# Kernel tuning notes

Hardware: AMD Instinct MI355X
Metric: run time of the kernel (lower is better)

## Reference

```python
import jax, jax.numpy as jnp
import numpy as np

N_E = 8192
E_DIM = 256
BETA = 0.25

def setup_inputs() -> dict:
    key = jax.random.key(0)
    k1, k2 = jax.random.split(key)
    z = jax.random.normal(k1, (2, E_DIM, 8, 32, 32), dtype=jnp.float32)
    # nn.Embedding init: uniform(-1/n_e, 1/n_e)
    codebook = jax.random.uniform(k2, (N_E, E_DIM), dtype=jnp.float32,
                                  minval=-1.0 / N_E, maxval=1.0 / N_E)
    return {"z": z, "codebook": codebook}

def reference(z, codebook):
    # b c d h w -> b d h w c
    z_t = jnp.transpose(z, (0, 2, 3, 4, 1))  # [B,D,H,W,C]
    zf = z_t.reshape(-1, E_DIM)               # [N, C]
    # squared-distance: ||z||^2 + ||e||^2 - 2 z.e^T
    d = (jnp.sum(zf * zf, axis=1, keepdims=True)
         + jnp.sum(codebook * codebook, axis=1)
         - 2.0 * jnp.matmul(zf, codebook.T))  # [N, n_e]
    idx = jnp.argmin(d, axis=1)                # [N]
    z_q = codebook[idx].reshape(z_t.shape)     # [B,D,H,W,C]
    sg = jax.lax.stop_gradient
    loss = jnp.mean((sg(z_q) - z_t) ** 2) + BETA * jnp.mean((z_q - sg(z_t)) ** 2)
    # straight-through estimator
    z_q_st = z_t + sg(z_q - z_t)
    z_q_out = jnp.transpose(z_q_st, (0, 4, 1, 2, 3))  # [B,C,D,H,W]
    # perplexity (no-grad stats)
    min_encodings = jax.nn.one_hot(idx, N_E, dtype=jnp.float32)  # [N, n_e]
    e_mean = jnp.mean(min_encodings, axis=0)
    perplexity = jnp.exp(-jnp.sum(e_mean * jnp.log(e_mean + 1e-10)))
    return (z_q_out, loss, perplexity, min_encodings, idx)
```

## Files before the change

### kernel.cpp

```cpp
#include <hip/hip_runtime.h>

typedef _Float16 half8 __attribute__((ext_vector_type(8)));
typedef float floatx4 __attribute__((ext_vector_type(4)));

#define DEVI __device__ __forceinline__
#define AS1 __attribute__((address_space(1)))
#define AS3 __attribute__((address_space(3)))
#define GLL(gp, lp) __builtin_amdgcn_global_load_lds((const AS1 void*)(gp), (AS3 void*)(lp), 16, 0, 0)
#define VM0 asm volatile("s_waitcnt vmcnt(0)" ::: "memory")
#define VM2 asm volatile("s_waitcnt vmcnt(2)" ::: "memory")
#define BAR __builtin_amdgcn_s_barrier()

namespace {
constexpr int C_   = 256;
constexpr int DHW_ = 8192;
constexpr int N_   = 16384;
constexpr int NE_  = 8192;
constexpr int K_   = 256;

constexpr size_t LOSS_OFF  = 4194304;
constexpr size_t PERP_OFF  = 4194305;
constexpr size_t ENC_OFF   = 4194306;
constexpr size_t ENC_N     = 134217728ull;
constexpr size_t IDX_OFF   = ENC_OFF + ENC_N;

constexpr size_t SCR_ZH   = 480ull << 20;
constexpr size_t SCR_ZL   = 488ull << 20;
constexpr size_t SCR_EH   = 496ull << 20;
constexpr size_t SCR_EL   = 500ull << 20;
constexpr size_t SCR_ZZ   = 504ull << 20;
constexpr size_t SCR_KEY  = 505ull << 20;
constexpr size_t SCR_PART = 506ull << 20;
constexpr size_t SCR_HIST = 507ull << 20;

constexpr int NLOSS_BLOCKS = 2048;

constexpr size_t ZFILL_PER_BLK = 61440;
constexpr size_t TAIL_START    = 8 + 8192ull * ZFILL_PER_BLK;
constexpr size_t TAIL_F4       = (536870904ull - TAIL_START) / 16;
}


__global__ void vq_split(const float* __restrict__ z, const float* __restrict__ cb,
                         _Float16* __restrict__ ZHb, _Float16* __restrict__ ZLb,
                         _Float16* __restrict__ EHb, _Float16* __restrict__ ELb,
                         float* __restrict__ zz, unsigned long long* __restrict__ keys,
                         int* __restrict__ hist) {
    __shared__ float tile[64][260];
    int t = threadIdx.x;
    if (blockIdx.x < 512) {
        int n0 = blockIdx.x * 32;
        int b  = n0 >> 13;
        int d0 = n0 & 8191;
        const float* zb = z + (size_t)b * (C_ * DHW_) + d0;
        int j5 = t & 31, cg8 = t >> 5;
        for (int cc = 0; cc < 256; cc += 8) {
            int c = cc + cg8;
            tile[j5][c] = zb[(size_t)c * DHW_ + j5];
        }
        __syncthreads();
        int tl = n0 >> 8, r0 = n0 & 255;
        #pragma unroll
        for (int it = 0; it < 4; ++it) {
            int rid = it * 8 + cg8;
            half8 h, l;
            #pragma unroll
            for (int e = 0; e < 8; ++e) {
                float v = tile[j5][rid * 8 + e];
                _Float16 hh = (_Float16)v;
                h[e] = hh;
                l[e] = (_Float16)((v - (float)hh) * 2048.0f);
            }
            size_t off = ((size_t)(tl * 8 + (rid >> 2))) * 8192
                       + (size_t)(rid & 3) * 2048 + (size_t)(r0 + j5) * 8;
            *(half8*)(ZHb + off) = h;
            *(half8*)(ZLb + off) = l;
        }
        if (t < 32) {
            float tot[2];
            for (int h2 = 0; h2 < 2; ++h2) {
                float r8[8];
                #pragma unroll
                for (int k = 0; k < 8; ++k) { float x = tile[t][h2*128 + k]; r8[k] = x * x; }
                for (int i = 8; i < 128; i += 8) {
                    #pragma unroll
                    for (int k = 0; k < 8; ++k) { float x = tile[t][h2*128 + i + k]; r8[k] += x * x; }
                }
                tot[h2] = ((r8[0]+r8[1]) + (r8[2]+r8[3])) + ((r8[4]+r8[5]) + (r8[6]+r8[7]));
            }
            zz[n0 + t] = tot[0] + tot[1];
        }
        if (blockIdx.x < 64) keys[blockIdx.x * 256 + t] = ~0ull;
        else if (blockIdx.x < 96) hist[(blockIdx.x - 64) * 256 + t] = 0;
    } else {
        int j = t & 63, grp = t >> 6;
        int j0 = (blockIdx.x - 512) * 64;
        for (int i = 0; i < 64; ++i)
            tile[i][t] = cb[(size_t)(j0 + i) * K_ + t] * 65536.0f;
        __syncthreads();
        int tl = j0 >> 7, r0 = j0 & 127;
        #pragma unroll
        for (int it = 0; it < 8; ++it) {
            int rid = it * 4 + grp;
            half8 h, l;
            #pragma unroll
            for (int e = 0; e < 8; ++e) {
                float v = tile[j][rid * 8 + e];
                _Float16 hh = (_Float16)v;
                h[e] = hh;
                l[e] = (_Float16)((v - (float)hh) * 2048.0f);
            }
            size_t off = ((size_t)(tl * 8 + (rid >> 2))) * 4096
                       + (size_t)(rid & 3) * 1024 + (size_t)(r0 + j) * 8;
            *(half8*)(EHb + off) = h;
            *(half8*)(ELb + off) = l;
        }
    }
}


DEVI void stage_chunk(const char* zh, const char* zl, const char* eh, const char* el,
                      char* b, int t, int c) {
    #pragma unroll
    for (int i = 0; i < 2; ++i) {
        int f = i * 256 + t;
        int ao = (f >> 7) * 4096 + (f & 127) * 16;
        int eo = (f >> 7) * 2048 + (f & 127) * 16;
        GLL(zh + (size_t)c * 16384 + ao, b + f * 16);
        GLL(zl + (size_t)c * 16384 + ao, b + 8192 + f * 16);
        GLL(eh + (size_t)c * 8192 + eo, b + 16384 + f * 16);
        GLL(el + (size_t)c * 8192 + eo, b + 24576 + f * 16);
    }
}

DEVI void zfill2(char* zb, int t, int r0) {
    floatx4 z4 = {0.f, 0.f, 0.f, 0.f};
    __builtin_nontemporal_store(z4, (floatx4*)(zb + (size_t)r0 * 4096 + t * 16));
    __builtin_nontemporal_store(z4, (floatx4*)(zb + (size_t)(r0 + 1) * 4096 + t * 16));
}

DEVI void compute_chunk(const char* b, int wm, int wn, int g, int rr,
                        floatx4 (&acc_a)[4][4], floatx4 (&acc_b)[4][4]) {
    const char* Ab = b + g * 2048;
    const char* Bb = b + 16384 + g * 2048;
    half8 azh[4], azl[4], beh[4], bel[4];
    #pragma unroll
    for (int f = 0; f < 4; ++f) {
        int row = wm * 64 + f * 16 + rr;
        azh[f] = *(const half8*)(Ab + row * 16);
        azl[f] = *(const half8*)(Ab + 8192 + row * 16);
        int col = wn * 64 + f * 16 + rr;
        beh[f] = *(const half8*)(Bb + col * 16);
        bel[f] = *(const half8*)(Bb + 8192 + col * 16);
    }
    __builtin_amdgcn_s_setprio(1);
    #pragma unroll
    for (int fi = 0; fi < 4; ++fi)
        #pragma unroll
        for (int fj = 0; fj < 4; ++fj) {
            acc_a[fi][fj] = __builtin_amdgcn_mfma_f32_16x16x32_f16(azh[fi], beh[fj], acc_a[fi][fj], 0, 0, 0);
            acc_b[fi][fj] = __builtin_amdgcn_mfma_f32_16x16x32_f16(azl[fi], beh[fj], acc_b[fi][fj], 0, 0, 0);
            acc_b[fi][fj] = __builtin_amdgcn_mfma_f32_16x16x32_f16(azh[fi], bel[fj], acc_b[fi][fj], 0, 0, 0);
        }
    __builtin_amdgcn_s_setprio(0);
}

__launch_bounds__(256, 2)
__global__ void vq_gemm_argmin(const _Float16* __restrict__ ZHb, const _Float16* __restrict__ ZLb,
                               const _Float16* __restrict__ EHb, const _Float16* __restrict__ ELb,
                               const float* __restrict__ zz,
                               unsigned long long* __restrict__ keys,
                               char* __restrict__ zfill) {
    __shared__ _Float16 lds[2][16384];
    __shared__ unsigned long long rowmin[128];

    int orig = blockIdx.x;
    int xcd = orig & 7;
    int loc = orig >> 3;
    int bm = xcd * 16 + (loc & 15);
    int bn = loc >> 4;
    int m0 = bm * 128, n0v = bn * 128;

    int t = threadIdx.x;
    int lane = t & 63, wid = t >> 6;
    int wm = wid >> 1, wn = wid & 1;
    int g = lane >> 4, rr = lane & 15;

    const char* zh = (const char*)ZHb + (size_t)(bm >> 1) * 131072 + (size_t)(bm & 1) * 2048;
    const char* zl = (const char*)ZLb + (size_t)(bm >> 1) * 131072 + (size_t)(bm & 1) * 2048;
    const char* eh = (const char*)EHb + (size_t)bn * 65536;
    const char* el = (const char*)ELb + (size_t)bn * 65536;
    char* zb = zfill + (size_t)orig * ZFILL_PER_BLK;

    floatx4 acc_a[4][4], acc_b[4][4];
    #pragma unroll
    for (int i = 0; i < 4; ++i)
        #pragma unroll
        for (int jj = 0; jj < 4; ++jj) {
            acc_a[i][jj] = (floatx4){0.f, 0.f, 0.f, 0.f};
            acc_b[i][jj] = (floatx4){0.f, 0.f, 0.f, 0.f};
        }

    char* L0 = (char*)lds[0];
    char* L1 = (char*)lds[1];

    stage_chunk(zh, zl, eh, el, L0, t, 0);
    VM0; BAR;
    stage_chunk(zh, zl, eh, el, L1, t, 1); zfill2(zb, t, 0);  compute_chunk(L0, wm, wn, g, rr, acc_a, acc_b); VM2; BAR;
    stage_chunk(zh, zl, eh, el, L0, t, 2); zfill2(zb, t, 2);  compute_chunk(L1, wm, wn, g, rr, acc_a, acc_b); VM2; BAR;
    stage_chunk(zh, zl, eh, el, L1, t, 3); zfill2(zb, t, 4);  compute_chunk(L0, wm, wn, g, rr, acc_a, acc_b); VM2; BAR;
    stage_chunk(zh, zl, eh, el, L0, t, 4); zfill2(zb, t, 6);  compute_chunk(L1, wm, wn, g, rr, acc_a, acc_b); VM2; BAR;
    stage_chunk(zh, zl, eh, el, L1, t, 5); zfill2(zb, t, 8);  compute_chunk(L0, wm, wn, g, rr, acc_a, acc_b); VM2; BAR;
    stage_chunk(zh, zl, eh, el, L0, t, 6); zfill2(zb, t, 10); compute_chunk(L1, wm, wn, g, rr, acc_a, acc_b); VM2; BAR;
    stage_chunk(zh, zl, eh, el, L1, t, 7); zfill2(zb, t, 12); compute_chunk(L0, wm, wn, g, rr, acc_a, acc_b); VM2; BAR;
    {
        floatx4 z4 = {0.f, 0.f, 0.f, 0.f};
        __builtin_nontemporal_store(z4, (floatx4*)(zb + 14ull * 4096 + t * 16));
    }
    compute_chunk(L1, wm, wn, g, rr, acc_a, acc_b);

    if (t < 128) rowmin[t] = ~0ull;
    __syncthreads();

    constexpr float S_A = 1.0f / 65536.0f;
    constexpr float S_B = 1.0f / 134217728.0f;
    #pragma unroll
    for (int fi = 0; fi < 4; ++fi) {
        #pragma unroll
        for (int r = 0; r < 4; ++r) {
            int rowl = wm * 64 + fi * 16 + g * 4 + r;
            float zzv = zz[m0 + rowl];
            unsigned long long best = ~0ull;
            #pragma unroll
            for (int fj = 0; fj < 4; ++fj) {
                float dot = acc_a[fi][fj][r] * S_A + acc_b[fi][fj][r] * S_B;
                float d = zzv - 2.0f * dot;
                unsigned int db = __float_as_uint(d);
                unsigned int jg = (unsigned)(n0v + wn * 64 + fj * 16 + rr);
                unsigned long long key = ((unsigned long long)db << 32) | jg;
                if (key < best) best = key;
            }
            #pragma unroll
            for (int s = 1; s < 16; s <<= 1) {
                unsigned long long o = __shfl_xor(best, s, 64);
                if (o < best) best = o;
            }
            if (rr == 0) atomicMin(&rowmin[rowl], best);
        }
    }
    __syncthreads();
    if (t < 128) atomicMin(&keys[m0 + t], rowmin[t]);
}

__global__ void vq_zq_loss(const float* __restrict__ z, const float* __restrict__ cb,
                           const unsigned long long* __restrict__ keys,
                           float* __restrict__ out0, float* __restrict__ parts,
                           float* __restrict__ out_idx, int* __restrict__ hist) {
    size_t i0 = ((size_t)blockIdx.x * 256 + threadIdx.x) * 8;
    int c   = (int)((i0 >> 13) & 255);
    int b   = (int)(i0 >> 21);
    int dhw = (int)(i0 & 8191);
    int nb  = b * DHW_ + dhw;
    int jj[8];
    #pragma unroll
    for (int e = 0; e < 8; ++e)
        jj[e] = (int)(unsigned)(keys[nb + e] & 0xFFFFFFFFull);
    float ls = 0.f;
    #pragma unroll
    for (int e = 0; e < 8; ++e) {
        float zq = cb[(size_t)jj[e] * K_ + c];
        float zt = z[i0 + e];
        float diff = zq - zt;
        out0[i0 + e] = zt + diff;
        ls += diff * diff;
    }
    if (c == 0) {
        #pragma unroll
        for (int e = 0; e < 8; ++e) {
            out_idx[nb + e] = (float)jj[e];
            atomicAdd(&hist[jj[e]], 1);
        }
    }
    __shared__ float red[256];
    red[threadIdx.x] = ls;
    __syncthreads();
    for (int s = 128; s > 0; s >>= 1) {
        if (threadIdx.x < (unsigned)s) red[threadIdx.x] += red[threadIdx.x + s];
        __syncthreads();
    }
    if (threadIdx.x == 0) parts[blockIdx.x] = red[0];
}

__global__ void vq_finalize_scalars(const float* __restrict__ parts,
                                    const int* __restrict__ hist,
                                    float* __restrict__ out) {
    __shared__ double dred[256];
    int t = threadIdx.x;
    double ent = 0.0;
    for (int i = t; i < NE_; i += 256) {
        float em = (float)hist[i] * (1.0f / 16384.0f);
        float term = em * logf(em + 1e-10f);
        ent += (double)term;
    }
    dred[t] = ent;
    __syncthreads();
    for (int s = 128; s > 0; s >>= 1) {
        if (t < s) dred[t] += dred[t + s];
        __syncthreads();
    }
    double entr = 0.0;
    if (t == 0) entr = dred[0];
    __syncthreads();
    double ls = 0.0;
    for (int i = t; i < NLOSS_BLOCKS; i += 256) ls += (double)parts[i];
    dred[t] = ls;
    __syncthreads();
    for (int s = 128; s > 0; s >>= 1) {
        if (t < s) dred[t] += dred[t + s];
        __syncthreads();
    }
    if (t == 0) {
        double m = dred[0] / 4194304.0;
        float m1 = (float)m;
        out[LOSS_OFF] = m1 + 0.25f * m1;
        out[PERP_OFF] = (float)exp(-entr);
    }
}

__global__ void vq_zero_tail(char* __restrict__ encb) {
    size_t i = (size_t)blockIdx.x * 256 + threadIdx.x;
    floatx4 z4 = {0.f, 0.f, 0.f, 0.f};
    char* base = encb + TAIL_START;
    for (size_t k = i; k < TAIL_F4; k += 131072)
        *(floatx4*)(base + k * 16) = z4;
    if (i == 0) {
        float2 z2 = {0.f, 0.f};
        *(float2*)encb = z2;
        *(float2*)(encb + 536870904ull) = z2;
    }
}

__global__ void vq_write_ones(const float* __restrict__ idxf, float* __restrict__ enc) {
    int n = blockIdx.x * 256 + threadIdx.x;
    enc[(size_t)n * NE_ + (int)idxf[n]] = 1.0f;
}

extern "C" void kernel_launch(void* const* d_in, const int* in_sizes, int n_in,
                              void* d_out, int out_size, void* d_ws, size_t ws_size,
                              hipStream_t stream) {
    const float* z  = (const float*)d_in[0];
    const float* cb = (const float*)d_in[1];
    float* out = (float*)d_out;

    char* scr = (char*)(((uintptr_t)(out + ENC_OFF) + 255) & ~(uintptr_t)255);
    _Float16* ZHb = (_Float16*)(scr + SCR_ZH);
    _Float16* ZLb = (_Float16*)(scr + SCR_ZL);
    _Float16* EHb = (_Float16*)(scr + SCR_EH);
    _Float16* ELb = (_Float16*)(scr + SCR_EL);
    float* zz = (float*)(scr + SCR_ZZ);
    unsigned long long* keys = (unsigned long long*)(scr + SCR_KEY);
    float* parts = (float*)(scr + SCR_PART);
    int* hist = (int*)(scr + SCR_HIST);
    float* out_idx = out + IDX_OFF;
    float* enc = out + ENC_OFF;
    char* encb = (char*)enc;

    vq_split<<<640, 256, 0, stream>>>(z, cb, ZHb, ZLb, EHb, ELb, zz, keys, hist);
    vq_gemm_argmin<<<8192, 256, 0, stream>>>(ZHb, ZLb, EHb, ELb, zz, keys, encb + 8);
    vq_zq_loss<<<NLOSS_BLOCKS, 256, 0, stream>>>(z, cb, keys, out, parts, out_idx, hist);
    vq_finalize_scalars<<<1, 256, 0, stream>>>(parts, hist, out);
    vq_zero_tail<<<512, 256, 0, stream>>>(encb);
    vq_write_ones<<<64, 256, 0, stream>>>(out_idx, enc);
}
```

Baseline: 296.6 us.

## Load Z fragments directly from global memory, stage only codebook in LDS

The A-operand (z hi/lo halves) is no longer staged through LDS. Each wave reads its fragments straight from global memory into registers, while only the codebook tiles are double-buffered in LDS. This halves LDS footprint and LDS traffic, which may allow better occupancy. The cost is that each wave now fetches Z from global/L2 with per-iteration latency exposed before the MFMAs, and the wait is tightened to vmcnt(0).

Measured after the change: 307.8 us. +3.8%, slower.

```diff
diff --git a/kernel.cpp b/kernel.cpp
--- a/kernel.cpp
+++ b/kernel.cpp
@@ -8,7 +8,6 @@
 #define AS3 __attribute__((address_space(3)))
 #define GLL(gp, lp) __builtin_amdgcn_global_load_lds((const AS1 void*)(gp), (AS3 void*)(lp), 16, 0, 0)
 #define VM0 asm volatile("s_waitcnt vmcnt(0)" ::: "memory")
-#define VM2 asm volatile("s_waitcnt vmcnt(2)" ::: "memory")
 #define BAR __builtin_amdgcn_s_barrier()
 
 namespace {
@@ -119,40 +118,40 @@
 }
 
 
-DEVI void stage_chunk(const char* zh, const char* zl, const char* eh, const char* el,
-                      char* b, int t, int c) {
+DEVI void stage_chunkB(const char* eh, const char* el, char* b, int t, int c) {
     #pragma unroll
     for (int i = 0; i < 2; ++i) {
         int f = i * 256 + t;
-        int ao = (f >> 7) * 4096 + (f & 127) * 16;
         int eo = (f >> 7) * 2048 + (f & 127) * 16;
-        GLL(zh + (size_t)c * 16384 + ao, b + f * 16);
-        GLL(zl + (size_t)c * 16384 + ao, b + 8192 + f * 16);
-        GLL(eh + (size_t)c * 8192 + eo, b + 16384 + f * 16);
-        GLL(el + (size_t)c * 8192 + eo, b + 24576 + f * 16);
-    }
-}
-
-DEVI void zfill2(char* zb, int t, int r0) {
-    floatx4 z4 = {0.f, 0.f, 0.f, 0.f};
-    __builtin_nontemporal_store(z4, (floatx4*)(zb + (size_t)r0 * 4096 + t * 16));
-    __builtin_nontemporal_store(z4, (floatx4*)(zb + (size_t)(r0 + 1) * 4096 + t * 16));
-}
-
-DEVI void compute_chunk(const char* b, int wm, int wn, int g, int rr,
-                        floatx4 (&acc_a)[4][4], floatx4 (&acc_b)[4][4]) {
-    const char* Ab = b + g * 2048;
-    const char* Bb = b + 16384 + g * 2048;
+        GLL(eh + (size_t)c * 8192 + eo, b + f * 16);
+        GLL(el + (size_t)c * 8192 + eo, b + 8192 + f * 16);
+    }
+}
+
+DEVI void gemm_iter(const char* zh, const char* zl, int c,
+                    const char* Lc, const char* eh, const char* el, char* Ln, bool last,
+                    char* zb, int r0, int nfill,
+                    int wm, int wn, int g, int rr, int t,
+                    floatx4 (&acc_a)[4][4], floatx4 (&acc_b)[4][4]) {
+    const char* Bb = Lc + g * 2048;
     half8 azh[4], azl[4], beh[4], bel[4];
+    size_t abase = (size_t)c * 16384 + (size_t)g * 4096;
     #pragma unroll
     for (int f = 0; f < 4; ++f) {
         int row = wm * 64 + f * 16 + rr;
-        azh[f] = *(const half8*)(Ab + row * 16);
-        azl[f] = *(const half8*)(Ab + 8192 + row * 16);
+        azh[f] = *(const half8*)(zh + abase + row * 16);
+        azl[f] = *(const half8*)(zl + abase + row * 16);
+    }
+    #pragma unroll
+    for (int f = 0; f < 4; ++f) {
         int col = wn * 64 + f * 16 + rr;
         beh[f] = *(const half8*)(Bb + col * 16);
         bel[f] = *(const half8*)(Bb + 8192 + col * 16);
     }
+    if (!last) stage_chunkB(eh, el, Ln, t, c + 1);
+    floatx4 z4 = {0.f, 0.f, 0.f, 0.f};
+    if (nfill >= 1) __builtin_nontemporal_store(z4, (floatx4*)(zb + (size_t)r0 * 4096 + t * 16));
+    if (nfill >= 2) __builtin_nontemporal_store(z4, (floatx4*)(zb + (size_t)(r0 + 1) * 4096 + t * 16));
     __builtin_amdgcn_s_setprio(1);
     #pragma unroll
     for (int fi = 0; fi < 4; ++fi)
@@ -171,7 +170,7 @@
                                const float* __restrict__ zz,
                                unsigned long long* __restrict__ keys,
                                char* __restrict__ zfill) {
-    __shared__ _Float16 lds[2][16384];
+    __shared__ _Float16 lds[2][8192];
     __shared__ unsigned long long rowmin[128];
 
     int orig = blockIdx.x;
@@ -204,20 +203,16 @@
     char* L0 = (char*)lds[0];
     char* L1 = (char*)lds[1];
 
-    stage_chunk(zh, zl, eh, el, L0, t, 0);
+    stage_chunkB(eh, el, L0, t, 0);
     VM0; BAR;
-    stage_chunk(zh, zl, eh, el, L1, t, 1); zfill2(zb, t, 0);  compute_chunk(L0, wm, wn, g, rr, acc_a, acc_b); VM2; BAR;
-    stage_chunk(zh, zl, eh, el, L0, t, 2); zfill2(zb, t, 2);  compute_chunk(L1, wm, wn, g, rr, acc_a, acc_b); VM2; BAR;
-    stage_chunk(zh, zl, eh, el, L1, t, 3); zfill2(zb, t, 4);  compute_chunk(L0, wm, wn, g, rr, acc_a, acc_b); VM2; BAR;
-    stage_chunk(zh, zl, eh, el, L0, t, 4); zfill2(zb, t, 6);  compute_chunk(L1, wm, wn, g, rr, acc_a, acc_b); VM2; BAR;
-    stage_chunk(zh, zl, eh, el, L1, t, 5); zfill2(zb, t, 8);  compute_chunk(L0, wm, wn, g, rr, acc_a, acc_b); VM2; BAR;
-    stage_chunk(zh, zl, eh, el, L0, t, 6); zfill2(zb, t, 10); compute_chunk(L1, wm, wn, g, rr, acc_a, acc_b); VM2; BAR;
-    stage_chunk(zh, zl, eh, el, L1, t, 7); zfill2(zb, t, 12); compute_chunk(L0, wm, wn, g, rr, acc_a, acc_b); VM2; BAR;
-    {
-        floatx4 z4 = {0.f, 0.f, 0.f, 0.f};
-        __builtin_nontemporal_store(z4, (floatx4*)(zb + 14ull * 4096 + t * 16));
-    }
-    compute_chunk(L1, wm, wn, g, rr, acc_a, acc_b);
+    gemm_iter(zh, zl, 0, L0, eh, el, L1, false, zb, 0,  2, wm, wn, g, rr, t, acc_a, acc_b); VM0; BAR;
+    gemm_iter(zh, zl, 1, L1, eh, el, L0, false, zb, 2,  2, wm, wn, g, rr, t, acc_a, acc_b); VM0; BAR;
+    gemm_iter(zh, zl, 2, L0, eh, el, L1, false, zb, 4,  2, wm, wn, g, rr, t, acc_a, acc_b); VM0; BAR;
+    gemm_iter(zh, zl, 3, L1, eh, el, L0, false, zb, 6,  2, wm, wn, g, rr, t, acc_a, acc_b); VM0; BAR;
+    gemm_iter(zh, zl, 4, L0, eh, el, L1, false, zb, 8,  2, wm, wn, g, rr, t, acc_a, acc_b); VM0; BAR;
+    gemm_iter(zh, zl, 5, L1, eh, el, L0, false, zb, 10, 2, wm, wn, g, rr, t, acc_a, acc_b); VM0; BAR;
+    gemm_iter(zh, zl, 6, L0, eh, el, L1, false, zb, 12, 2, wm, wn, g, rr, t, acc_a, acc_b); VM0; BAR;
+    gemm_iter(zh, zl, 7, L1, eh, el, L0, true,  zb, 14, 1, wm, wn, g, rr, t, acc_a, acc_b);
 
     if (t < 128) rowmin[t] = ~0ull;
     __syncthreads();
```

## Use 256x128 tiles with 512 threads and triple-buffered LDS pipeline

Applied to the files above, without the earlier changes.

Enlarges the GEMM+argmin block tile from 128x128 to 256x128 using 8 waves, halving the grid, so each codebook chunk staged in LDS is reused across more rows. The LDS ring grows from two buffers to three, so loads are issued two chunks ahead with relaxed vmcnt waits, hiding more global latency. The encoding zero-fill is redistributed to the wider blocks. The cost is much more LDS per block (about 144KB plus the row-min array), which may limit occupancy to one block per CU.

Result: no change. 291.9 us (-1.6%).

```diff
diff --git a/kernel.cpp b/kernel.cpp
--- a/kernel.cpp
+++ b/kernel.cpp
@@ -7,7 +7,8 @@
 #define AS1 __attribute__((address_space(1)))
 #define AS3 __attribute__((address_space(3)))
 #define GLL(gp, lp) __builtin_amdgcn_global_load_lds((const AS1 void*)(gp), (AS3 void*)(lp), 16, 0, 0)
-#define VM0 asm volatile("s_waitcnt vmcnt(0)" ::: "memory")
+#define VM6 asm volatile("s_waitcnt vmcnt(6)" ::: "memory")
+#define VM8 asm volatile("s_waitcnt vmcnt(8)" ::: "memory")
 #define VM2 asm volatile("s_waitcnt vmcnt(2)" ::: "memory")
 #define BAR __builtin_amdgcn_s_barrier()
 
@@ -35,8 +36,8 @@
 
 constexpr int NLOSS_BLOCKS = 2048;
 
-constexpr size_t ZFILL_PER_BLK = 61440;
-constexpr size_t TAIL_START    = 8 + 8192ull * ZFILL_PER_BLK;
+constexpr size_t ZFILL_PER_BLK = 122880;
+constexpr size_t TAIL_START    = 8 + 4096ull * ZFILL_PER_BLK;
 constexpr size_t TAIL_F4       = (536870904ull - TAIL_START) / 16;
 }
 
@@ -123,32 +124,37 @@
                       char* b, int t, int c) {
     #pragma unroll
     for (int i = 0; i < 2; ++i) {
-        int f = i * 256 + t;
-        int ao = (f >> 7) * 4096 + (f & 127) * 16;
-        int eo = (f >> 7) * 2048 + (f & 127) * 16;
+        int f = i * 512 + t;
+        int ao = (f >> 8) * 4096 + (f & 255) * 16;
         GLL(zh + (size_t)c * 16384 + ao, b + f * 16);
-        GLL(zl + (size_t)c * 16384 + ao, b + 8192 + f * 16);
-        GLL(eh + (size_t)c * 8192 + eo, b + 16384 + f * 16);
-        GLL(el + (size_t)c * 8192 + eo, b + 24576 + f * 16);
-    }
+    }
+    #pragma unroll
+    for (int i = 0; i < 2; ++i) {
+        int f = i * 512 + t;
+        int ao = (f >> 8) * 4096 + (f & 255) * 16;
+        GLL(zl + (size_t)c * 16384 + ao, b + 16384 + f * 16);
+    }
+    int eo = (t >> 7) * 2048 + (t & 127) * 16;
+    GLL(eh + (size_t)c * 8192 + eo, b + 32768 + t * 16);
+    GLL(el + (size_t)c * 8192 + eo, b + 40960 + t * 16);
 }
 
 DEVI void zfill2(char* zb, int t, int r0) {
     floatx4 z4 = {0.f, 0.f, 0.f, 0.f};
-    __builtin_nontemporal_store(z4, (floatx4*)(zb + (size_t)r0 * 4096 + t * 16));
-    __builtin_nontemporal_store(z4, (floatx4*)(zb + (size_t)(r0 + 1) * 4096 + t * 16));
+    __builtin_nontemporal_store(z4, (floatx4*)(zb + (size_t)r0 * 8192 + t * 16));
+    __builtin_nontemporal_store(z4, (floatx4*)(zb + (size_t)(r0 + 1) * 8192 + t * 16));
 }
 
 DEVI void compute_chunk(const char* b, int wm, int wn, int g, int rr,
                         floatx4 (&acc_a)[4][4], floatx4 (&acc_b)[4][4]) {
-    const char* Ab = b + g * 2048;
-    const char* Bb = b + 16384 + g * 2048;
+    const char* Ab = b + g * 4096;
+    const char* Bb = b + 32768 + g * 2048;
     half8 azh[4], azl[4], beh[4], bel[4];
     #pragma unroll
     for (int f = 0; f < 4; ++f) {
         int row = wm * 64 + f * 16 + rr;
         azh[f] = *(const half8*)(Ab + row * 16);
-        azl[f] = *(const half8*)(Ab + 8192 + row * 16);
+        azl[f] = *(const half8*)(Ab + 16384 + row * 16);
         int col = wn * 64 + f * 16 + rr;
         beh[f] = *(const half8*)(Bb + col * 16);
         bel[f] = *(const half8*)(Bb + 8192 + col * 16);
@@ -165,29 +171,29 @@
     __builtin_amdgcn_s_setprio(0);
 }
 
-__launch_bounds__(256, 2)
+__launch_bounds__(512, 2)
 __global__ void vq_gemm_argmin(const _Float16* __restrict__ ZHb, const _Float16* __restrict__ ZLb,
                                const _Float16* __restrict__ EHb, const _Float16* __restrict__ ELb,
                                const float* __restrict__ zz,
                                unsigned long long* __restrict__ keys,
                                char* __restrict__ zfill) {
-    __shared__ _Float16 lds[2][16384];
-    __shared__ unsigned long long rowmin[128];
+    __shared__ _Float16 lds[3][24576];
+    __shared__ unsigned long long rowmin[256];
 
     int orig = blockIdx.x;
     int xcd = orig & 7;
     int loc = orig >> 3;
-    int bm = xcd * 16 + (loc & 15);
-    int bn = loc >> 4;
-    int m0 = bm * 128, n0v = bn * 128;
+    int bm = xcd * 8 + (loc & 7);
+    int bn = loc >> 3;
+    int m0 = bm * 256, n0v = bn * 128;
 
     int t = threadIdx.x;
     int lane = t & 63, wid = t >> 6;
     int wm = wid >> 1, wn = wid & 1;
     int g = lane >> 4, rr = lane & 15;
 
-    const char* zh = (const char*)ZHb + (size_t)(bm >> 1) * 131072 + (size_t)(bm & 1) * 2048;
-    const char* zl = (const char*)ZLb + (size_t)(bm >> 1) * 131072 + (size_t)(bm & 1) * 2048;
+    const char* zh = (const char*)ZHb + (size_t)bm * 131072;
+    const char* zl = (const char*)ZLb + (size_t)bm * 131072;
     const char* eh = (const char*)EHb + (size_t)bn * 65536;
     const char* el = (const char*)ELb + (size_t)bn * 65536;
     char* zb = zfill + (size_t)orig * ZFILL_PER_BLK;
@@ -203,23 +209,25 @@
 
     char* L0 = (char*)lds[0];
     char* L1 = (char*)lds[1];
+    char* L2 = (char*)lds[2];
 
     stage_chunk(zh, zl, eh, el, L0, t, 0);
-    VM0; BAR;
-    stage_chunk(zh, zl, eh, el, L1, t, 1); zfill2(zb, t, 0);  compute_chunk(L0, wm, wn, g, rr, acc_a, acc_b); VM2; BAR;
-    stage_chunk(zh, zl, eh, el, L0, t, 2); zfill2(zb, t, 2);  compute_chunk(L1, wm, wn, g, rr, acc_a, acc_b); VM2; BAR;
-    stage_chunk(zh, zl, eh, el, L1, t, 3); zfill2(zb, t, 4);  compute_chunk(L0, wm, wn, g, rr, acc_a, acc_b); VM2; BAR;
-    stage_chunk(zh, zl, eh, el, L0, t, 4); zfill2(zb, t, 6);  compute_chunk(L1, wm, wn, g, rr, acc_a, acc_b); VM2; BAR;
-    stage_chunk(zh, zl, eh, el, L1, t, 5); zfill2(zb, t, 8);  compute_chunk(L0, wm, wn, g, rr, acc_a, acc_b); VM2; BAR;
-    stage_chunk(zh, zl, eh, el, L0, t, 6); zfill2(zb, t, 10); compute_chunk(L1, wm, wn, g, rr, acc_a, acc_b); VM2; BAR;
-    stage_chunk(zh, zl, eh, el, L1, t, 7); zfill2(zb, t, 12); compute_chunk(L0, wm, wn, g, rr, acc_a, acc_b); VM2; BAR;
+    stage_chunk(zh, zl, eh, el, L1, t, 1);
+    VM6; BAR;
+    stage_chunk(zh, zl, eh, el, L2, t, 2); zfill2(zb, t, 0);  compute_chunk(L0, wm, wn, g, rr, acc_a, acc_b); VM8; BAR;
+    stage_chunk(zh, zl, eh, el, L0, t, 3); zfill2(zb, t, 2);  compute_chunk(L1, wm, wn, g, rr, acc_a, acc_b); VM8; BAR;
+    stage_chunk(zh, zl, eh, el, L1, t, 4); zfill2(zb, t, 4);  compute_chunk(L2, wm, wn, g, rr, acc_a, acc_b); VM8; BAR;
+    stage_chunk(zh, zl, eh, el, L2, t, 5); zfill2(zb, t, 6);  compute_chunk(L0, wm, wn, g, rr, acc_a, acc_b); VM8; BAR;
+    stage_chunk(zh, zl, eh, el, L0, t, 6); zfill2(zb, t, 8);  compute_chunk(L1, wm, wn, g, rr, acc_a, acc_b); VM8; BAR;
+    stage_chunk(zh, zl, eh, el, L1, t, 7); zfill2(zb, t, 10); compute_chunk(L2, wm, wn, g, rr, acc_a, acc_b); VM8; BAR;
+    zfill2(zb, t, 12);                                        compute_chunk(L0, wm, wn, g, rr, acc_a, acc_b); VM2; BAR;
     {
         floatx4 z4 = {0.f, 0.f, 0.f, 0.f};
-        __builtin_nontemporal_store(z4, (floatx4*)(zb + 14ull * 4096 + t * 16));
+        __builtin_nontemporal_store(z4, (floatx4*)(zb + 14ull * 8192 + t * 16));
     }
     compute_chunk(L1, wm, wn, g, rr, acc_a, acc_b);
 
-    if (t < 128) rowmin[t] = ~0ull;
+    if (t < 256) rowmin[t] = ~0ull;
     __syncthreads();
 
     constexpr float S_A = 1.0f / 65536.0f;
@@ -249,7 +257,7 @@
         }
     }
     __syncthreads();
-    if (t < 128) atomicMin(&keys[m0 + t], rowmin[t]);
+    if (t < 256) atomicMin(&keys[m0 + t], rowmin[t]);
 }
 
 __global__ void vq_zq_loss(const float* __restrict__ z, const float* __restrict__ cb,
@@ -366,7 +374,7 @@
     char* encb = (char*)enc;
 
     vq_split<<<640, 256, 0, stream>>>(z, cb, ZHb, ZLb, EHb, ELb, zz, keys, hist);
-    vq_gemm_argmin<<<8192, 256, 0, stream>>>(ZHb, ZLb, EHb, ELb, zz, keys, encb + 8);
+    vq_gemm_argmin<<<4096, 512, 0, stream>>>(ZHb, ZLb, EHb, ELb, zz, keys, encb + 8);
     vq_zq_loss<<<NLOSS_BLOCKS, 256, 0, stream>>>(z, cb, keys, out, parts, out_idx, hist);
     vq_finalize_scalars<<<1, 256, 0, stream>>>(parts, hist, out);
     vq_zero_tail<<<512, 256, 0, stream>>>(encb);
```
